# Kernel optimization log

Measured on AMD Instinct MI355X. Metric: run time of the kernel, lower is better.

The kernel has to match this reference:

```python
import jax, jax.numpy as jnp
import numpy as np


def setup_inputs() -> dict:
    key = jax.random.key(0)
    ks = jax.random.split(key, 8)
    nf, nloc, nnei, ng2 = 1, 1024, 128, 32
    nd, nh = 32, 4
    g2 = jax.random.normal(ks[0], (nf, nloc, nnei, ng2), jnp.float32)
    h2 = jax.random.normal(ks[1], (nf, nloc, nnei, 3), jnp.float32)
    sw = jax.random.uniform(ks[2], (nf, nloc, nnei), jnp.float32)
    nlist_mask = jax.random.randint(ks[3], (nf, nloc, nnei), 0, 2).astype(jnp.int32)
    w_qk = jax.random.normal(ks[4], (ng2, nd * 2 * nh), jnp.float32) / np.sqrt(ng2)
    w_v = jax.random.normal(ks[5], (ng2, ng2 * nh), jnp.float32) / np.sqrt(ng2)
    w_head = jax.random.normal(ks[6], (ng2 * nh, ng2), jnp.float32) / np.sqrt(ng2 * nh)
    b_head = jnp.zeros((ng2,), jnp.float32)
    w_eqhead = jax.random.normal(ks[7], (nh, 1), jnp.float32) / np.sqrt(nh)
    return dict(g2=g2, h2=h2, sw=sw, w_qk=w_qk, w_v=w_v, w_head=w_head,
                b_head=b_head, w_eqhead=w_eqhead, nlist_mask=nlist_mask)


def reference(g2, h2, sw, w_qk, w_v, w_head, b_head, w_eqhead, nlist_mask):
    ATTNW_SHIFT = 20.0
    nf, nloc, nnei, ng2 = g2.shape
    nh = w_eqhead.shape[0]
    nd = w_qk.shape[1] // (2 * nh)
    mask = nlist_mask.astype(bool)

    # --- Atten2Map: build gated, smoothed multi-head attention A[b,i,h,q,k] ---
    qk = (g2 @ w_qk).reshape(nf, nloc, nnei, nd, 2 * nh)
    qk = jnp.transpose(qk, (0, 1, 4, 2, 3))            # (b, i, 2nh, nnei, nd)
    q, k = qk[:, :, :nh], qk[:, :, nh:]
    A = jnp.einsum('bihqd,bihkd->bihqk', q, k) / jnp.sqrt(jnp.float32(nd))
    h2ht = jnp.einsum('biqc,bikc->biqk', h2, h2)       # h2 @ h2^T (gate, pre-scale)
    A = A * h2ht[:, :, None]                            # has_gate=True
    swq = sw[:, :, None, :, None]
    swk = sw[:, :, None, None, :]
    A = (A + ATTNW_SHIFT) * swq * swk - ATTNW_SHIFT     # smooth shift
    A = jax.nn.softmax(A, axis=-1)
    A = jnp.where(mask[:, :, None, None, :], A, 0.0)   # attnw_mask (keys)
    A = jnp.where(mask[:, :, None, :, None], A, 0.0)   # attnw_mask_c (queries)
    A = A * swq * swk
    A = A * (h2ht / jnp.sqrt(jnp.float32(3.0)))[:, :, None]  # * h2h2t/sqrt(3)

    # --- Atten2MultiHeadApply: invariant g2 update ---
    g2v = (g2 @ w_v).reshape(nf, nloc, nnei, ng2, nh)
    out_g = jnp.einsum('bihqk,bikgh->biqgh', A, g2v).reshape(nf, nloc, nnei, ng2 * nh)
    g2_out = out_g @ w_head + b_head

    # --- Atten2EquiVarApply: equivariant h2 update ---
    out_h = jnp.einsum('bihqk,bikc->biqch', A, h2)      # (b, i, nnei, 3, nh)
    h2_out = (out_h @ w_eqhead)[..., 0]                 # (b, i, nnei, 3)
    return g2_out, h2_out
```

## Files before the change

### kernel.cpp

```cpp
#include <hip/hip_runtime.h>


typedef __bf16 v8bf __attribute__((ext_vector_type(8)));
typedef float  v4f  __attribute__((ext_vector_type(4)));
typedef unsigned u32x2 __attribute__((ext_vector_type(2)));
typedef unsigned u32x4 __attribute__((ext_vector_type(4)));

__device__ __forceinline__ float b2f(unsigned short b) {
    union { unsigned u; float f; } x; x.u = ((unsigned)b) << 16; return x.f;
}
__device__ __forceinline__ unsigned short f2b(float f) {
    union { float f; unsigned u; } x; x.f = f;
    unsigned r = x.u + 0x7FFFu + ((x.u >> 16) & 1u);
    return (unsigned short)(r >> 16);
}
struct HL { unsigned short hi, lo; };
__device__ __forceinline__ HL splitbf(float f) {
    HL r; r.hi = f2b(f); r.lo = f2b(f - b2f(r.hi)); return r;
}
__device__ __forceinline__ unsigned pk2(unsigned short lo, unsigned short hi) {
    return ((unsigned)hi << 16) | (unsigned)lo;
}
__device__ __forceinline__ v8bf mkv8(unsigned a, unsigned b, unsigned c, unsigned d) {
    u32x4 x = {a, b, c, d};
    return __builtin_bit_cast(v8bf, x);
}
__device__ __forceinline__ float hwe(const float* h2s, int kn,
                                     float hq0, float hq1, float hq2) {
    const v4f hk = *(const v4f*)(h2s + kn * 4);
    return fmaf(hq2, hk[2], fmaf(hq1, hk[1], hq0 * hk[0]));
}

#define MF(a,b,c) __builtin_amdgcn_mfma_f32_16x16x32_bf16((a),(b),(c),0,0,0)
#define FENCE() asm volatile("" ::: "memory")

#if __has_builtin(__builtin_amdgcn_exp2f)
#define EXP2(x) __builtin_amdgcn_exp2f(x)
#else
#define EXP2(x) __expf((x) * 0.6931471805599453f)
#endif

#define MSH (-28.853900817779268f)

#define G2H 0
#define G2L 4096
#define G2T 8192
#define NQH 12544
#define NQL 16640
#define H2T 20736
#define PQ  21280
#define SM_U16 25376

#define RPERM(C) ((((C) >> 2) & 1) * 16 + (((C) >> 3) << 2) + ((C) & 3))

#define CC_(a,b) a##b
#define CC(a,b) CC_(a,b)

#define LD8(NM, IDX) \
    HL CC(NM,0) = splitbf(IDX(0)), CC(NM,1) = splitbf(IDX(1)), \
       CC(NM,2) = splitbf(IDX(2)), CC(NM,3) = splitbf(IDX(3)), \
       CC(NM,4) = splitbf(IDX(4)), CC(NM,5) = splitbf(IDX(5)), \
       CC(NM,6) = splitbf(IDX(6)), CC(NM,7) = splitbf(IDX(7));
#define HI8(NM) mkv8(pk2(CC(NM,0).hi, CC(NM,1).hi), pk2(CC(NM,2).hi, CC(NM,3).hi), \
                     pk2(CC(NM,4).hi, CC(NM,5).hi), pk2(CC(NM,6).hi, CC(NM,7).hi))
#define LO8(NM) mkv8(pk2(CC(NM,0).lo, CC(NM,1).lo), pk2(CC(NM,2).lo, CC(NM,3).lo), \
                     pk2(CC(NM,4).lo, CC(NM,5).lo), pk2(CC(NM,6).lo, CC(NM,7).lo))

__global__ __launch_bounds__(256, 3) void repformer_kernel(
    const float* __restrict__ g2, const float* __restrict__ h2,
    const float* __restrict__ sw, const float* __restrict__ wqk,
    const float* __restrict__ wv, const float* __restrict__ wh,
    const float* __restrict__ bh, const float* __restrict__ weq,
    const int*   __restrict__ nmask, float* __restrict__ out)
{
    __shared__ __align__(16) unsigned short sm[SM_U16];
    __shared__ __align__(16) float smf[772];
    float* h2s = smf;
    float* sws = smf + 512;
    float* es  = smf + 640;
    float* wqs = smf + 768;

    const int t    = threadIdx.x;
    const int i    = blockIdx.x;
    const int lane = t & 63;
    const int wv4  = t >> 6;
    const int quad = lane >> 4;
    const int n16  = lane & 15;
    const int h    = wv4;

    {
        const float4* src = (const float4*)(g2 + (size_t)i * 4096);
        #pragma unroll
        for (int j = 0; j < 4; j++) {
            int idx = j * 256 + t;
            float4 v = src[idx];
            HL a0 = splitbf(v.x), a1 = splitbf(v.y), a2 = splitbf(v.z), a3 = splitbf(v.w);
            int k = idx >> 3, c0 = (idx & 7) * 4;
            int swz = k * 32 + (c0 ^ ((k & 3) << 3));
            *(u32x2*)(sm + G2H + swz) = (u32x2){pk2(a0.hi, a1.hi), pk2(a2.hi, a3.hi)};
            *(u32x2*)(sm + G2L + swz) = (u32x2){pk2(a0.lo, a1.lo), pk2(a2.lo, a3.lo)};
            sm[G2T + RPERM(c0 + 0) * 136 + k] = a0.hi;
            sm[G2T + RPERM(c0 + 1) * 136 + k] = a1.hi;
            sm[G2T + RPERM(c0 + 2) * 136 + k] = a2.hi;
            sm[G2T + RPERM(c0 + 3) * 136 + k] = a3.hi;
        }
    }
    for (int e = t; e < 384; e += 256) {
        float f = h2[(size_t)i * 384 + e];
        int k = e / 3, c = e - k * 3;
        h2s[k * 4 + c] = f;
        sm[H2T + c * 136 + k] = f2b(f);
    }
    if (t < 128) {
        sm[H2T + 3 * 136 + t] = 0;
        float s = sw[i * 128 + t];
        sws[t] = s;
        es[t]  = (nmask[i * 128 + t] != 0) ? s : 0.0f;
    }
    if (t < 4) wqs[t] = weq[t];

#define WKI(J) wqk[(mt * 16 + n16) * 256 + (quad * 8 + (J)) * 8 + 4 + h]
#define WVI(J) wv[(mt * 16 + n16) * 128 + (quad * 8 + (J)) * 4 + h]
#define WQI(J) wqk[(nt * 16 + n16) * 256 + (quad * 8 + (J)) * 8 + h]
#define WHI(J) wh[((quad * 8 + (J)) * 4 + h) * 32 + nt * 16 + n16]
    #pragma unroll 1
    for (int mt = 0; mt < 2; mt++) {
        LD8(ak, WKI)
        LD8(av, WVI)
        const v8bf akh = HI8(ak), akl = LO8(ak);
        const v8bf avh = HI8(av), avl = LO8(av);
        FENCE();
        #pragma unroll 1
        for (int nt = 0; nt < 2; nt++) {
            LD8(bq, WQI)
            LD8(bw, WHI)
            const v8bf bqh = HI8(bq), bql = LO8(bq);
            const v8bf bhh = HI8(bw), bhl = LO8(bw);
            FENCE();
            const v4f z = {0.f, 0.f, 0.f, 0.f};
            v4f c1 = MF(akh, bqh, MF(akl, bqh, MF(akh, bql, z)));
            #pragma unroll
            for (int r = 0; r < 4; r++) {
                HL s1 = splitbf(c1[r]);
                int x    = mt * 16 + quad * 4 + r;
                int rowp = RPERM(x);
                int addr = h * 1024 + rowp * 32 + ((nt * 16 + n16) ^ ((rowp & 3) << 3));
                sm[NQH + addr] = s1.hi; sm[NQL + addr] = s1.lo;
            }
            v4f c2 = MF(avh, bhh, MF(avl, bhh, MF(avh, bhl, z)));
            #pragma unroll
            for (int r = 0; r < 4; r++) {
                int o  = nt * 16 + n16;
                int cw = mt * 16 + quad * 4 + r;
                sm[PQ + h * 1024 + o * 32 + (cw ^ ((o & 3) << 3))] = f2b(c2[r]);
            }
            FENCE();
        }
    }
    __syncthreads();

    {
        int kcol = t & 127;
        int cb = (t >> 7) * 16;
        float ek = es[kcol];
        #pragma unroll
        for (int c = 0; c < 16; c++) {
            int idx = G2T + (cb + c) * 136 + kcol;
            sm[idx] = f2b(b2f(sm[idx]) * ek);
        }
        if (t < 128) {
            #pragma unroll
            for (int c = 0; c < 3; c++) {
                int idx = H2T + c * 136 + t;
                sm[idx] = f2b(b2f(sm[idx]) * es[t]);
            }
        }
    }
    __syncthreads();

    const int hr = (n16 < 3) ? n16 : 3;
    float* outg = out;
    float* outh = out + 4194304;
    const float bias0 = bh[n16];
    const float bias1 = bh[16 + n16];
    const int qo = (quad * 8) ^ ((n16 & 3) << 3);
    const int rowbase = ((n16 >> 2) << 3) + (n16 & 3);
    const unsigned short* g2t0 = sm + G2T + n16 * 136;
    const unsigned short* g2t1 = sm + G2T + (16 + n16) * 136;
    const unsigned short* h2tp = sm + H2T + hr * 136;

#define KSSTEP(KS, HWA, HWB) { \
    const int rowA = (KS) * 32 + rowbase; \
    const v8bf ah0 = *(const v8bf*)(sm + G2H + rowA * 32 + qo); \
    const v8bf al0 = *(const v8bf*)(sm + G2L + rowA * 32 + qo); \
    const v8bf ah1 = *(const v8bf*)(sm + G2H + (rowA + 4) * 32 + qo); \
    const v8bf al1 = *(const v8bf*)(sm + G2L + (rowA + 4) * 32 + qo); \
    const v4f st0 = MF(ah0, ql, MF(al0, qh, MF(ah0, qh, vz))); \
    const v4f st1 = MF(ah1, ql, MF(al1, qh, MF(ah1, qh, vz))); \
    const v4f swkA = *(const v4f*)(sws + (KS) * 32 + quad * 8); \
    const v4f swkB = *(const v4f*)(sws + (KS) * 32 + quad * 8 + 4); \
    const float p0 = EXP2(fmaf(fmaf(st0[0], (HWA)[0], swq20E), swkA[0], MSH)); \
    const float p1 = EXP2(fmaf(fmaf(st0[1], (HWA)[1], swq20E), swkA[1], MSH)); \
    const float p2 = EXP2(fmaf(fmaf(st0[2], (HWA)[2], swq20E), swkA[2], MSH)); \
    const float p3 = EXP2(fmaf(fmaf(st0[3], (HWA)[3], swq20E), swkA[3], MSH)); \
    const float p4 = EXP2(fmaf(fmaf(st1[0], (HWB)[0], swq20E), swkB[0], MSH)); \
    const float p5 = EXP2(fmaf(fmaf(st1[1], (HWB)[1], swq20E), swkB[1], MSH)); \
    const float p6 = EXP2(fmaf(fmaf(st1[2], (HWB)[2], swq20E), swkB[2], MSH)); \
    const float p7 = EXP2(fmaf(fmaf(st1[3], (HWB)[3], swq20E), swkB[3], MSH)); \
    sum += ((p0 + p1) + (p2 + p3)) + ((p4 + p5) + (p6 + p7)); \
    const v8bf pv = mkv8(pk2(f2b(p0 * (HWA)[0]), f2b(p1 * (HWA)[1])), \
                         pk2(f2b(p2 * (HWA)[2]), f2b(p3 * (HWA)[3])), \
                         pk2(f2b(p4 * (HWB)[0]), f2b(p5 * (HWB)[1])), \
                         pk2(f2b(p6 * (HWB)[2]), f2b(p7 * (HWB)[3]))); \
    T0  = MF(*(const v8bf*)(g2t0 + (KS) * 32 + quad * 8), pv, T0); \
    T1  = MF(*(const v8bf*)(g2t1 + (KS) * 32 + quad * 8), pv, T1); \
    ohl = MF(*(const v8bf*)(h2tp + (KS) * 32 + quad * 8), pv, ohl); \
    FENCE(); \
}

    #pragma unroll 1
    for (int sl = 0; sl < 2; sl++) {
        const int s = 2 * wv4 + sl;
        const int q = s * 16 + n16;
        const v8bf gfh = *(const v8bf*)(sm + G2H + q * 32 + qo);
        const v8bf gfl = *(const v8bf*)(sm + G2L + q * 32 + qo);
        const float swq    = sws[q];
        const float mq     = (es[q] != 0.0f) ? 1.0f : 0.0f;
        const float swq20E = swq * 28.853900817779268f;
        const float kq     = 0.17677669529663687f * 1.4426950408889634f * swq;
        const float hq0 = h2s[q * 4 + 0] * kq;
        const float hq1 = h2s[q * 4 + 1] * kq;
        const float hq2 = h2s[q * 4 + 2] * kq;
#define HW4(T8) (v4f){ hwe(h2s, ((T8) >> 1) * 32 + quad * 8 + ((T8) & 1) * 4 + 0, hq0, hq1, hq2), \
                       hwe(h2s, ((T8) >> 1) * 32 + quad * 8 + ((T8) & 1) * 4 + 1, hq0, hq1, hq2), \
                       hwe(h2s, ((T8) >> 1) * 32 + quad * 8 + ((T8) & 1) * 4 + 2, hq0, hq1, hq2), \
                       hwe(h2s, ((T8) >> 1) * 32 + quad * 8 + ((T8) & 1) * 4 + 3, hq0, hq1, hq2) }
        const v4f hw0 = HW4(0), hw1 = HW4(1), hw2 = HW4(2), hw3 = HW4(3);
        const v4f hw4 = HW4(4), hw5 = HW4(5), hw6 = HW4(6), hw7 = HW4(7);
        v4f og0 = {0.f, 0.f, 0.f, 0.f}, og1 = og0, ohacc = og0;
        FENCE();

        #pragma unroll 1
        for (int hd = 0; hd < 4; hd++) {
            const v4f vz = {0.f, 0.f, 0.f, 0.f};
            const unsigned short* nqh = sm + NQH + hd * 1024;
            const unsigned short* nql = sm + NQL + hd * 1024;
            const v8bf nh0 = *(const v8bf*)(nqh + n16 * 32 + qo);
            const v8bf nl0 = *(const v8bf*)(nql + n16 * 32 + qo);
            const v8bf nh1 = *(const v8bf*)(nqh + (16 + n16) * 32 + qo);
            const v8bf nl1 = *(const v8bf*)(nql + (16 + n16) * 32 + qo);
            v4f c0t = MF(nh0, gfl, MF(nl0, gfh, MF(nh0, gfh, vz)));
            v4f c1t = MF(nh1, gfl, MF(nl1, gfh, MF(nh1, gfh, vz)));
            FENCE();
            HL qa0 = splitbf(c0t[0]), qa1 = splitbf(c0t[1]);
            HL qa2 = splitbf(c0t[2]), qa3 = splitbf(c0t[3]);
            HL qb0 = splitbf(c1t[0]), qb1 = splitbf(c1t[1]);
            HL qb2 = splitbf(c1t[2]), qb3 = splitbf(c1t[3]);
            const v8bf qh = mkv8(pk2(qa0.hi, qa1.hi), pk2(qa2.hi, qa3.hi),
                                 pk2(qb0.hi, qb1.hi), pk2(qb2.hi, qb3.hi));
            const v8bf ql = mkv8(pk2(qa0.lo, qa1.lo), pk2(qa2.lo, qa3.lo),
                                 pk2(qb0.lo, qb1.lo), pk2(qb2.lo, qb3.lo));
            FENCE();
            v4f T0 = vz, T1 = vz, ohl = vz;
            float sum = 0.f;
            KSSTEP(0, hw0, hw1)
            KSSTEP(1, hw2, hw3)
            KSSTEP(2, hw4, hw5)
            KSSTEP(3, hw6, hw7)
            sum += __shfl_xor(sum, 16, 64);
            sum += __shfl_xor(sum, 32, 64);
            const float scale = mq * 2.2638092f * __builtin_amdgcn_rcpf(sum);
            const v8bf ta = mkv8(pk2(f2b(scale * T0[0]), f2b(scale * T0[1])),
                                 pk2(f2b(scale * T0[2]), f2b(scale * T0[3])),
                                 pk2(f2b(scale * T1[0]), f2b(scale * T1[1])),
                                 pk2(f2b(scale * T1[2]), f2b(scale * T1[3])));
            const unsigned short* wp = sm + PQ + hd * 1024;
            og0 = MF(ta, *(const v8bf*)(wp + n16 * 32 + qo), og0);
            og1 = MF(ta, *(const v8bf*)(wp + (16 + n16) * 32 + qo), og1);
            const float ws = wqs[hd] * scale;
            ohacc[0] = fmaf(ws, ohl[0], ohacc[0]);
            ohacc[1] = fmaf(ws, ohl[1], ohacc[1]);
            ohacc[2] = fmaf(ws, ohl[2], ohacc[2]);
            ohacc[3] = fmaf(ws, ohl[3], ohacc[3]);
            FENCE();
        }

        const int qg = i * 128 + s * 16;
        #pragma unroll
        for (int r = 0; r < 4; r++) {
            outg[(size_t)(qg + quad * 4 + r) * 32 + n16]      = og0[r] + bias0;
            outg[(size_t)(qg + quad * 4 + r) * 32 + 16 + n16] = og1[r] + bias1;
        }
        if (quad == 0) {
            #pragma unroll
            for (int r = 0; r < 3; r++)
                outh[(size_t)(qg + n16) * 3 + r] = ohacc[r];
        }
    }
}

extern "C" void kernel_launch(void* const* d_in, const int* in_sizes, int n_in,
                              void* d_out, int out_size, void* d_ws, size_t ws_size,
                              hipStream_t stream) {
    const float* g2  = (const float*)d_in[0];
    const float* h2  = (const float*)d_in[1];
    const float* sw  = (const float*)d_in[2];
    const float* wqk = (const float*)d_in[3];
    const float* wv  = (const float*)d_in[4];
    const float* wh  = (const float*)d_in[5];
    const float* bh  = (const float*)d_in[6];
    const float* weq = (const float*)d_in[7];
    const int*   nm  = (const int*)d_in[8];
    int nloc = in_sizes[0] / (128 * 32);
    repformer_kernel<<<nloc, 256, 0, stream>>>(g2, h2, sw, wqk, wv, wh, bh, weq, nm, (float*)d_out);
}
```

Measured before the change: 147.7 us.

## Use hardware bf16 conversion, improve LDS swizzle key, relax compiler fences

Replaces the manual round-to-nearest bf16 conversion with the native __bf16 cast, which lets the compiler emit packed hardware converts on gfx950. It also changes the LDS XOR swizzle key to mix bits 3-4 of the row, aiming to cut bank conflicts in the MFMA operand reads. Several compiler fences in the inner loop are removed or moved so the scheduler can interleave more freely. The new swizzle must match exactly on the write and read sides, and the fewer fences may raise register pressure.

```diff
diff --git a/kernel.cpp b/kernel.cpp
--- a/kernel.cpp
+++ b/kernel.cpp
@@ -9,17 +9,23 @@
 __device__ __forceinline__ float b2f(unsigned short b) {
     union { unsigned u; float f; } x; x.u = ((unsigned)b) << 16; return x.f;
 }
-__device__ __forceinline__ unsigned short f2b(float f) {
-    union { float f; unsigned u; } x; x.f = f;
-    unsigned r = x.u + 0x7FFFu + ((x.u >> 16) & 1u);
-    return (unsigned short)(r >> 16);
+__device__ __forceinline__ unsigned short fb(float f) {
+    return __builtin_bit_cast(unsigned short, (__bf16)f);
 }
 struct HL { unsigned short hi, lo; };
 __device__ __forceinline__ HL splitbf(float f) {
-    HL r; r.hi = f2b(f); r.lo = f2b(f - b2f(r.hi)); return r;
+    HL r; r.hi = fb(f); r.lo = fb(f - b2f(r.hi)); return r;
 }
 __device__ __forceinline__ unsigned pk2(unsigned short lo, unsigned short hi) {
     return ((unsigned)hi << 16) | (unsigned)lo;
+}
+__device__ __forceinline__ unsigned cvt2(float a, float b) {
+    return pk2(fb(a), fb(b));
+}
+__device__ __forceinline__ void sp2(float a, float b, unsigned& hi, unsigned& lo) {
+    __bf16 ah = (__bf16)a, bh = (__bf16)b;
+    hi = pk2(__builtin_bit_cast(unsigned short, ah), __builtin_bit_cast(unsigned short, bh));
+    lo = cvt2(a - (float)ah, b - (float)bh);
 }
 __device__ __forceinline__ v8bf mkv8(unsigned a, unsigned b, unsigned c, unsigned d) {
     u32x4 x = {a, b, c, d};
@@ -52,6 +58,7 @@
 #define SM_U16 25376
 
 #define RPERM(C) ((((C) >> 2) & 1) * 16 + (((C) >> 3) << 2) + ((C) & 3))
+#define KEY(R) ((((R) & 3) ^ (((R) >> 3) & 3)) << 3)
 
 #define CC_(a,b) a##b
 #define CC(a,b) CC_(a,b)
@@ -96,7 +103,7 @@
             float4 v = src[idx];
             HL a0 = splitbf(v.x), a1 = splitbf(v.y), a2 = splitbf(v.z), a3 = splitbf(v.w);
             int k = idx >> 3, c0 = (idx & 7) * 4;
-            int swz = k * 32 + (c0 ^ ((k & 3) << 3));
+            int swz = k * 32 + (c0 ^ KEY(k));
             *(u32x2*)(sm + G2H + swz) = (u32x2){pk2(a0.hi, a1.hi), pk2(a2.hi, a3.hi)};
             *(u32x2*)(sm + G2L + swz) = (u32x2){pk2(a0.lo, a1.lo), pk2(a2.lo, a3.lo)};
             sm[G2T + RPERM(c0 + 0) * 136 + k] = a0.hi;
@@ -109,7 +116,7 @@
         float f = h2[(size_t)i * 384 + e];
         int k = e / 3, c = e - k * 3;
         h2s[k * 4 + c] = f;
-        sm[H2T + c * 136 + k] = f2b(f);
+        sm[H2T + c * 136 + k] = fb(f);
     }
     if (t < 128) {
         sm[H2T + 3 * 136 + t] = 0;
@@ -144,7 +151,7 @@
                 HL s1 = splitbf(c1[r]);
                 int x    = mt * 16 + quad * 4 + r;
                 int rowp = RPERM(x);
-                int addr = h * 1024 + rowp * 32 + ((nt * 16 + n16) ^ ((rowp & 3) << 3));
+                int addr = h * 1024 + rowp * 32 + ((nt * 16 + n16) ^ KEY(rowp));
                 sm[NQH + addr] = s1.hi; sm[NQL + addr] = s1.lo;
             }
             v4f c2 = MF(avh, bhh, MF(avl, bhh, MF(avh, bhl, z)));
@@ -152,7 +159,7 @@
             for (int r = 0; r < 4; r++) {
                 int o  = nt * 16 + n16;
                 int cw = mt * 16 + quad * 4 + r;
-                sm[PQ + h * 1024 + o * 32 + (cw ^ ((o & 3) << 3))] = f2b(c2[r]);
+                sm[PQ + h * 1024 + o * 32 + (cw ^ KEY(o))] = fb(c2[r]);
             }
             FENCE();
         }
@@ -166,13 +173,13 @@
         #pragma unroll
         for (int c = 0; c < 16; c++) {
             int idx = G2T + (cb + c) * 136 + kcol;
-            sm[idx] = f2b(b2f(sm[idx]) * ek);
+            sm[idx] = fb(b2f(sm[idx]) * ek);
         }
         if (t < 128) {
             #pragma unroll
             for (int c = 0; c < 3; c++) {
                 int idx = H2T + c * 136 + t;
-                sm[idx] = f2b(b2f(sm[idx]) * es[t]);
+                sm[idx] = fb(b2f(sm[idx]) * es[t]);
             }
         }
     }
@@ -183,18 +190,20 @@
     float* outh = out + 4194304;
     const float bias0 = bh[n16];
     const float bias1 = bh[16 + n16];
-    const int qo = (quad * 8) ^ ((n16 & 3) << 3);
+    const int qo0 = (quad * 8) ^ KEY(n16);
+    const int qo1 = (quad * 8) ^ KEY(16 + n16);
     const int rowbase = ((n16 >> 2) << 3) + (n16 & 3);
+    const int qoK = (quad * 8) ^ KEY(rowbase);
     const unsigned short* g2t0 = sm + G2T + n16 * 136;
     const unsigned short* g2t1 = sm + G2T + (16 + n16) * 136;
     const unsigned short* h2tp = sm + H2T + hr * 136;
 
 #define KSSTEP(KS, HWA, HWB) { \
     const int rowA = (KS) * 32 + rowbase; \
-    const v8bf ah0 = *(const v8bf*)(sm + G2H + rowA * 32 + qo); \
-    const v8bf al0 = *(const v8bf*)(sm + G2L + rowA * 32 + qo); \
-    const v8bf ah1 = *(const v8bf*)(sm + G2H + (rowA + 4) * 32 + qo); \
-    const v8bf al1 = *(const v8bf*)(sm + G2L + (rowA + 4) * 32 + qo); \
+    const v8bf ah0 = *(const v8bf*)(sm + G2H + rowA * 32 + qoK); \
+    const v8bf al0 = *(const v8bf*)(sm + G2L + rowA * 32 + qoK); \
+    const v8bf ah1 = *(const v8bf*)(sm + G2H + (rowA + 4) * 32 + qoK); \
+    const v8bf al1 = *(const v8bf*)(sm + G2L + (rowA + 4) * 32 + qoK); \
     const v4f st0 = MF(ah0, ql, MF(al0, qh, MF(ah0, qh, vz))); \
     const v4f st1 = MF(ah1, ql, MF(al1, qh, MF(ah1, qh, vz))); \
     const v4f swkA = *(const v4f*)(sws + (KS) * 32 + quad * 8); \
@@ -208,22 +217,22 @@
     const float p6 = EXP2(fmaf(fmaf(st1[2], (HWB)[2], swq20E), swkB[2], MSH)); \
     const float p7 = EXP2(fmaf(fmaf(st1[3], (HWB)[3], swq20E), swkB[3], MSH)); \
     sum += ((p0 + p1) + (p2 + p3)) + ((p4 + p5) + (p6 + p7)); \
-    const v8bf pv = mkv8(pk2(f2b(p0 * (HWA)[0]), f2b(p1 * (HWA)[1])), \
-                         pk2(f2b(p2 * (HWA)[2]), f2b(p3 * (HWA)[3])), \
-                         pk2(f2b(p4 * (HWB)[0]), f2b(p5 * (HWB)[1])), \
-                         pk2(f2b(p6 * (HWB)[2]), f2b(p7 * (HWB)[3]))); \
+    const v8bf pv = mkv8(cvt2(p0 * (HWA)[0], p1 * (HWA)[1]), \
+                         cvt2(p2 * (HWA)[2], p3 * (HWA)[3]), \
+                         cvt2(p4 * (HWB)[0], p5 * (HWB)[1]), \
+                         cvt2(p6 * (HWB)[2], p7 * (HWB)[3])); \
     T0  = MF(*(const v8bf*)(g2t0 + (KS) * 32 + quad * 8), pv, T0); \
     T1  = MF(*(const v8bf*)(g2t1 + (KS) * 32 + quad * 8), pv, T1); \
     ohl = MF(*(const v8bf*)(h2tp + (KS) * 32 + quad * 8), pv, ohl); \
-    FENCE(); \
 }
 
     #pragma unroll 1
     for (int sl = 0; sl < 2; sl++) {
         const int s = 2 * wv4 + sl;
         const int q = s * 16 + n16;
-        const v8bf gfh = *(const v8bf*)(sm + G2H + q * 32 + qo);
-        const v8bf gfl = *(const v8bf*)(sm + G2L + q * 32 + qo);
+        const int qoq = (quad * 8) ^ KEY(q);
+        const v8bf gfh = *(const v8bf*)(sm + G2H + q * 32 + qoq);
+        const v8bf gfl = *(const v8bf*)(sm + G2L + q * 32 + qoq);
         const float swq    = sws[q];
         const float mq     = (es[q] != 0.0f) ? 1.0f : 0.0f;
         const float swq20E = swq * 28.853900817779268f;
@@ -245,38 +254,36 @@
             const v4f vz = {0.f, 0.f, 0.f, 0.f};
             const unsigned short* nqh = sm + NQH + hd * 1024;
             const unsigned short* nql = sm + NQL + hd * 1024;
-            const v8bf nh0 = *(const v8bf*)(nqh + n16 * 32 + qo);
-            const v8bf nl0 = *(const v8bf*)(nql + n16 * 32 + qo);
-            const v8bf nh1 = *(const v8bf*)(nqh + (16 + n16) * 32 + qo);
-            const v8bf nl1 = *(const v8bf*)(nql + (16 + n16) * 32 + qo);
+            const v8bf nh0 = *(const v8bf*)(nqh + n16 * 32 + qo0);
+            const v8bf nl0 = *(const v8bf*)(nql + n16 * 32 + qo0);
+            const v8bf nh1 = *(const v8bf*)(nqh + (16 + n16) * 32 + qo1);
+            const v8bf nl1 = *(const v8bf*)(nql + (16 + n16) * 32 + qo1);
             v4f c0t = MF(nh0, gfl, MF(nl0, gfh, MF(nh0, gfh, vz)));
             v4f c1t = MF(nh1, gfl, MF(nl1, gfh, MF(nh1, gfh, vz)));
-            FENCE();
-            HL qa0 = splitbf(c0t[0]), qa1 = splitbf(c0t[1]);
-            HL qa2 = splitbf(c0t[2]), qa3 = splitbf(c0t[3]);
-            HL qb0 = splitbf(c1t[0]), qb1 = splitbf(c1t[1]);
-            HL qb2 = splitbf(c1t[2]), qb3 = splitbf(c1t[3]);
-            const v8bf qh = mkv8(pk2(qa0.hi, qa1.hi), pk2(qa2.hi, qa3.hi),
-                                 pk2(qb0.hi, qb1.hi), pk2(qb2.hi, qb3.hi));
-            const v8bf ql = mkv8(pk2(qa0.lo, qa1.lo), pk2(qa2.lo, qa3.lo),
-                                 pk2(qb0.lo, qb1.lo), pk2(qb2.lo, qb3.lo));
-            FENCE();
+            unsigned qh0, qh1, qh2, qh3, ql0, ql1, ql2, ql3;
+            sp2(c0t[0], c0t[1], qh0, ql0);
+            sp2(c0t[2], c0t[3], qh1, ql1);
+            sp2(c1t[0], c1t[1], qh2, ql2);
+            sp2(c1t[2], c1t[3], qh3, ql3);
+            const v8bf qh = mkv8(qh0, qh1, qh2, qh3);
+            const v8bf ql = mkv8(ql0, ql1, ql2, ql3);
             v4f T0 = vz, T1 = vz, ohl = vz;
             float sum = 0.f;
             KSSTEP(0, hw0, hw1)
             KSSTEP(1, hw2, hw3)
+            FENCE();
             KSSTEP(2, hw4, hw5)
             KSSTEP(3, hw6, hw7)
             sum += __shfl_xor(sum, 16, 64);
             sum += __shfl_xor(sum, 32, 64);
             const float scale = mq * 2.2638092f * __builtin_amdgcn_rcpf(sum);
-            const v8bf ta = mkv8(pk2(f2b(scale * T0[0]), f2b(scale * T0[1])),
-                                 pk2(f2b(scale * T0[2]), f2b(scale * T0[3])),
-                                 pk2(f2b(scale * T1[0]), f2b(scale * T1[1])),
-                                 pk2(f2b(scale * T1[2]), f2b(scale * T1[3])));
+            const v8bf ta = mkv8(cvt2(scale * T0[0], scale * T0[1]),
+                                 cvt2(scale * T0[2], scale * T0[3]),
+                                 cvt2(scale * T1[0], scale * T1[1]),
+                                 cvt2(scale * T1[2], scale * T1[3]));
             const unsigned short* wp = sm + PQ + hd * 1024;
-            og0 = MF(ta, *(const v8bf*)(wp + n16 * 32 + qo), og0);
-            og1 = MF(ta, *(const v8bf*)(wp + (16 + n16) * 32 + qo), og1);
+            og0 = MF(ta, *(const v8bf*)(wp + n16 * 32 + qo0), og0);
+            og1 = MF(ta, *(const v8bf*)(wp + (16 + n16) * 32 + qo1), og1);
             const float ws = wqs[hd] * scale;
             ohacc[0] = fmaf(ws, ohl[0], ohacc[0]);
             ohacc[1] = fmaf(ws, ohl[1], ohacc[1]);
```

Result: faster. 144.1 us (-2.4%).
